# Kernel optimization log

Hardware: AMD Instinct MI355X
Metric: run time of the kernel (lower is better)

## Reference

```python
import jax, jax.numpy as jnp
import numpy as np

N, E, D_IN, D_H, G = 50000, 800000, 300, 128, 128


def gat_conv(x, src, dst, W, att_src, att_dst, bias):
    # PyG GATConv, heads=1, concat, negative_slope=0.2, self-loops already appended.
    h = x @ W                              # [N, F]
    a_s = h @ att_src                      # [N]
    a_d = h @ att_dst                      # [N]
    e = jax.nn.leaky_relu(a_s[src] + a_d[dst], 0.2)   # [E+N]
    m = jax.ops.segment_max(e, dst, num_segments=h.shape[0])
    ex = jnp.exp(e - m[dst])
    denom = jax.ops.segment_sum(ex, dst, num_segments=h.shape[0])
    alpha = ex / denom[dst]                # softmax over in-edges of each dst
    out = jax.ops.segment_sum(alpha[:, None] * h[src], dst, num_segments=h.shape[0])
    return out + bias


def setup_inputs() -> dict:
    key = jax.random.key(0)
    ks = jax.random.split(key, 12)
    x = jax.random.normal(ks[0], (N, D_IN), dtype=jnp.float32)
    edge_index = jax.random.randint(ks[1], (2, E), 0, N)
    batch = jnp.sort(jax.random.randint(ks[2], (N,), 0, G))
    pos = jax.random.randint(ks[3], (N,), 0, 2).astype(bool)
    s = 0.05
    W1 = jax.random.normal(ks[4], (D_IN, D_H), dtype=jnp.float32) * s
    as1 = jax.random.normal(ks[5], (D_H,), dtype=jnp.float32) * s
    ad1 = jax.random.normal(ks[6], (D_H,), dtype=jnp.float32) * s
    b1 = jnp.zeros((D_H,), dtype=jnp.float32)
    W2 = jax.random.normal(ks[7], (D_H, D_H), dtype=jnp.float32) * s
    as2 = jax.random.normal(ks[8], (D_H,), dtype=jnp.float32) * s
    ad2 = jax.random.normal(ks[9], (D_H,), dtype=jnp.float32) * s
    b2 = jnp.zeros((D_H,), dtype=jnp.float32)
    Wfc = jax.random.normal(ks[10], (D_H, 1), dtype=jnp.float32) * s
    bfc = jnp.zeros((1,), dtype=jnp.float32)
    return {"x": x, "edge_index": edge_index, "batch": batch, "pos": pos,
            "num_graphs": G, "W1": W1, "as1": as1, "ad1": ad1, "b1": b1,
            "W2": W2, "as2": as2, "ad2": ad2, "b2": b2, "Wfc": Wfc, "bfc": bfc}


def reference(x, edge_index, batch, pos, num_graphs, W1, as1, ad1, b1,
              W2, as2, ad2, b2, Wfc, bfc):
    n = x.shape[0]
    loop = jnp.arange(n)
    src = jnp.concatenate([edge_index[0], loop])
    dst = jnp.concatenate([edge_index[1], loop])
    h = gat_conv(x, src, dst, W1, as1, ad1, b1)
    h = jax.nn.gelu(h, approximate=False)
    # dropout is identity in eval mode
    h = gat_conv(h, src, dst, W2, as2, ad2, b2)   # [N, 128]
    # masked per-graph mean: logits[g] = mean over nodes with batch==g and pos
    w = pos.astype(h.dtype)                       # [N]
    sums = jax.ops.segment_sum(h * w[:, None], batch, num_segments=num_graphs)
    cnt = jax.ops.segment_sum(w, batch, num_segments=num_graphs)
    logits = sums / jnp.maximum(cnt, 1.0)[:, None]          # [G, 128]
    scores = (jax.nn.gelu(logits, approximate=False) @ Wfc + bfc).reshape(-1, num_graphs)
    return scores, logits
```

## Files before the change

### kernel.cpp

```cpp
#include <hip/hip_runtime.h>
#include <math.h>

#define NN 50000
#define EE 800000
#define DIN 300
#define DH 128
#define NG 128
#define RSIZE 6250

typedef __attribute__((ext_vector_type(8))) short short8;
typedef __attribute__((ext_vector_type(4))) float floatx4;

__device__ __forceinline__ float gelu_exact(float x) {
  return 0.5f * x * (1.0f + erff(x * 0.7071067811865476f));
}

__device__ __forceinline__ void split_bf16(float v, unsigned short& hi, unsigned short& lo) {
  unsigned int u = __float_as_uint(v);
  hi = (unsigned short)(u >> 16);
  float fh = __uint_as_float((unsigned int)hi << 16);
  lo = (unsigned short)(__float_as_uint(v - fh) >> 16);
}

__device__ __forceinline__ unsigned short f2bf_rne(float x) {
  unsigned int u = __float_as_uint(x);
  unsigned int r = (u + 0x7FFFu + ((u >> 16) & 1u)) >> 16;
  return (unsigned short)r;
}

__device__ __forceinline__ float bf_lo(unsigned u) { return __uint_as_float(u << 16); }
__device__ __forceinline__ float bf_hi(unsigned u) { return __uint_as_float(u & 0xFFFF0000u); }

__device__ __forceinline__ void async_ld16(void* lds, const void* g) {
  __builtin_amdgcn_global_load_lds(
      (const __attribute__((address_space(1))) unsigned int*)(unsigned long long)g,
      (__attribute__((address_space(3))) unsigned int*)(unsigned int)(unsigned long long)lds,
      16, 0, 0);
}


__global__ __launch_bounds__(256) void count_part_kernel(const int* __restrict__ ei,
                                                         int* __restrict__ deg,
                                                         int blocksPerRange) {
  const int r = blockIdx.x & 7;
  const int t = blockIdx.x >> 3;
  const int lo = r * RSIZE, hi = lo + RSIZE;
  const int total = EE + NN;
  const int step = blocksPerRange * 256;
  for (int e0 = t * 256; e0 < total; e0 += step) {
    int e = e0 + threadIdx.x;
    if (e < total) {
      int d = (e < EE) ? ei[EE + e] : (e - EE);
      if (d >= lo && d < hi) atomicAdd(&deg[d], 1);
    }
  }
}

__global__ __launch_bounds__(1024) void scan_part_kernel(const int* __restrict__ deg,
                                                         int* __restrict__ rowptr,
                                                         int* __restrict__ bsum) {
  __shared__ int wsum[16];
  const int tid = threadIdx.x;
  const int lane = tid & 63;
  const int wid = tid >> 6;
  int idx = blockIdx.x * 1024 + tid;
  int v = (idx < NN) ? deg[idx] : 0;
  int x = v;
#pragma unroll
  for (int d = 1; d < 64; d <<= 1) {
    int y = __shfl_up(x, d, 64);
    if (lane >= d) x += y;
  }
  if (lane == 63) wsum[wid] = x;
  __syncthreads();
  if (wid == 0) {
    int s = (lane < 16) ? wsum[lane] : 0;
#pragma unroll
    for (int d = 1; d < 16; d <<= 1) {
      int y = __shfl_up(s, d, 64);
      if (lane >= d) s += y;
    }
    if (lane < 16) wsum[lane] = s;
  }
  __syncthreads();
  int woff = (wid > 0) ? wsum[wid - 1] : 0;
  int incl = x + woff;
  if (idx < NN) rowptr[idx] = incl - v;
  if (tid == 1023) bsum[blockIdx.x] = incl;
}

__global__ __launch_bounds__(256) void scan_add_kernel(int* __restrict__ rowptr,
                                                       const int* __restrict__ bsum,
                                                       int* __restrict__ cursor, int nb) {
  __shared__ int boff_s[64];
  const int tid = threadIdx.x;
  if (tid < 64) {
    int lane = tid;
    int v = (lane < nb) ? bsum[lane] : 0;
    int x = v;
#pragma unroll
    for (int d = 1; d < 64; d <<= 1) {
      int y = __shfl_up(x, d, 64);
      if (lane >= d) x += y;
    }
    if (lane < nb) boff_s[lane] = x - v;
    if (lane == nb - 1) boff_s[nb] = x;
  }
  __syncthreads();
  int i = blockIdx.x * 256 + tid;
  if (i < NN) {
    int r = rowptr[i] + boff_s[i >> 10];
    rowptr[i] = r;
    cursor[i] = r;
  } else if (i == NN) {
    rowptr[NN] = boff_s[nb];
  }
}

__global__ __launch_bounds__(256) void scatter_part_kernel(const int* __restrict__ ei,
                                                           int* __restrict__ cursor,
                                                           int* __restrict__ colA,
                                                           int blocksPerRange) {
  const int r = blockIdx.x & 7;
  const int t = blockIdx.x >> 3;
  const int lo = r * RSIZE, hi = lo + RSIZE;
  const int total = EE + NN;
  const int step = blocksPerRange * 256;
  for (int e0 = t * 256; e0 < total; e0 += step) {
    int e = e0 + threadIdx.x;
    if (e < total) {
      int d = (e < EE) ? ei[EE + e] : (e - EE);
      if (d >= lo && d < hi) {
        int s = (e < EE) ? ei[e] : d;
        int p = atomicAdd(&cursor[d], 1);
        colA[p] = s;
      }
    }
  }
}


__global__ __launch_bounds__(256) void convert_bt2_kernel(
    const float* __restrict__ B1, unsigned short* __restrict__ B1h,
    unsigned short* __restrict__ B1l, int K1, int Kp1, int nblk1,
    const float* __restrict__ B2, unsigned short* __restrict__ B2h,
    unsigned short* __restrict__ B2l, int K2, int Kp2) {
  const float* B;
  unsigned short *Bh, *Bl;
  int K, Kpad, i;
  if ((int)blockIdx.x < nblk1) {
    B = B1; Bh = B1h; Bl = B1l; K = K1; Kpad = Kp1;
    i = blockIdx.x * 256 + threadIdx.x;
  } else {
    B = B2; Bh = B2h; Bl = B2l; K = K2; Kpad = Kp2;
    i = (blockIdx.x - nblk1) * 256 + threadIdx.x;
  }
  int n = i / Kpad, k = i % Kpad;
  if (n >= 128) return;
  float v = (k < K) ? B[(long)k * 128 + n] : 0.f;
  unsigned short h, l;
  split_bf16(v, h, l);
  Bh[(long)n * Kpad + k] = h;
  Bl[(long)n * Kpad + k] = l;
}


__global__ __launch_bounds__(256) void gemm_mfma_kernel(
    const float* __restrict__ A,
    const unsigned short* __restrict__ Bth, const unsigned short* __restrict__ Btl,
    unsigned short* __restrict__ C, int M, int K, int Kpad,
    const float* __restrict__ avs, const float* __restrict__ avd,
    float* __restrict__ aS, float* __restrict__ aD) {
  __shared__ __align__(16) unsigned short Bls[2][2][128 * 32];

  const int tid = threadIdx.x;
  const int lane = tid & 63;
  const int w = tid >> 6;
  const int q = lane >> 4;
  const int m16 = lane & 15;
  const int row0 = blockIdx.x * 64;
  const int myrow = row0 + w * 16 + m16;
  const bool rok = myrow < M;
  const long abase = (long)myrow * K;

  const int rl = lane >> 2, qq0 = lane & 3;
  const int nb0 = w * 16 + rl;
  const int nb1 = 64 + w * 16 + rl;
  const long boff0 = (long)nb0 * Kpad + (long)((qq0 ^ ((nb0 >> 1) & 3)) * 8);
  const long boff1 = (long)nb1 * Kpad + (long)((qq0 ^ ((nb1 >> 1) & 3)) * 8);

  floatx4 acc[8];
#pragma unroll
  for (int i = 0; i < 8; i++) acc[i] = (floatx4)(0.f);

  const int nsteps = Kpad / 32;

  float4 vA0, vA1, nA0, nA1;
  nA0 = nA1 = make_float4(0.f, 0.f, 0.f, 0.f);

  auto stageB = [&](int s, int nb) {
    const int k0 = s * 32;
    async_ld16(&Bls[nb][0][(w * 16) * 32], Bth + boff0 + k0);
    async_ld16(&Bls[nb][0][(64 + w * 16) * 32], Bth + boff1 + k0);
    async_ld16(&Bls[nb][1][(w * 16) * 32], Btl + boff0 + k0);
    async_ld16(&Bls[nb][1][(64 + w * 16) * 32], Btl + boff1 + k0);
  };
  auto loadA = [&](int s, float4& x0, float4& x1) {
    const int k0 = s * 32 + q * 8;
    x0 = make_float4(0.f, 0.f, 0.f, 0.f);
    x1 = x0;
    if (rok) {
      if (k0 + 4 <= K) x0 = *(const float4*)&A[abase + k0];
      if (k0 + 8 <= K) x1 = *(const float4*)&A[abase + k0 + 4];
    }
  };

  stageB(0, 0);
  loadA(0, vA0, vA1);
  __syncthreads();

  for (int s = 0; s < nsteps; s++) {
    const int cur = s & 1;
    if (s + 1 < nsteps) {
      stageB(s + 1, 1 ^ cur);
      loadA(s + 1, nA0, nA1);
    }
    float av[8] = {vA0.x, vA0.y, vA0.z, vA0.w, vA1.x, vA1.y, vA1.z, vA1.w};
    union {
      unsigned u[4];
      short8 s8;
    } Uh, Ul;
#pragma unroll
    for (int i = 0; i < 4; i++) {
      unsigned short ha, la, hb, lb;
      split_bf16(av[2 * i], ha, la);
      split_bf16(av[2 * i + 1], hb, lb);
      Uh.u[i] = (unsigned)ha | ((unsigned)hb << 16);
      Ul.u[i] = (unsigned)la | ((unsigned)lb << 16);
    }
    short8 afh = Uh.s8, afl = Ul.s8;
#pragma unroll
    for (int ct = 0; ct < 8; ct++) {
      int n = ct * 16 + m16;
      int qv = (q ^ ((n >> 1) & 3)) * 8;
      short8 bfh = *(const short8*)&Bls[cur][0][n * 32 + qv];
      short8 bfl = *(const short8*)&Bls[cur][1][n * 32 + qv];
      acc[ct] = __builtin_amdgcn_mfma_f32_16x16x32_bf16(afh, bfh, acc[ct], 0, 0, 0);
      acc[ct] = __builtin_amdgcn_mfma_f32_16x16x32_bf16(afh, bfl, acc[ct], 0, 0, 0);
      acc[ct] = __builtin_amdgcn_mfma_f32_16x16x32_bf16(afl, bfh, acc[ct], 0, 0, 0);
    }
    vA0 = nA0;
    vA1 = nA1;
    __syncthreads();
  }

  float avs_r[8], avd_r[8];
#pragma unroll
  for (int ct = 0; ct < 8; ct++) {
    avs_r[ct] = avs[ct * 16 + m16];
    avd_r[ct] = avd[ct * 16 + m16];
  }
#pragma unroll
  for (int reg = 0; reg < 4; reg++) {
    int grow = row0 + w * 16 + q * 4 + reg;
    bool ok = grow < M;
    float ps = 0.f, pd = 0.f;
#pragma unroll
    for (int ct = 0; ct < 8; ct++) {
      float c = acc[ct][reg];
      if (ok) C[(long)grow * 128 + ct * 16 + m16] = f2bf_rne(c);
      ps = fmaf(c, avs_r[ct], ps);
      pd = fmaf(c, avd_r[ct], pd);
    }
#pragma unroll
    for (int d = 1; d < 16; d <<= 1) {
      ps += __shfl_xor(ps, d, 64);
      pd += __shfl_xor(pd, d, 64);
    }
    if (m16 == 0 && ok) {
      aS[grow] = ps;
      aD[grow] = pd;
    }
  }
}


__global__ __launch_bounds__(256) void aggregate_kernel(const int* __restrict__ rowptr,
                                                        const int* __restrict__ colA,
                                                        const float* __restrict__ aS,
                                                        const float* __restrict__ aD,
                                                        const unsigned short* __restrict__ Hb,
                                                        const float* __restrict__ bias,
                                                        float* __restrict__ out,
                                                        int apply_gelu) {
  const int lane = threadIdx.x & 63;
  const int dst = blockIdx.x * 4 + (threadIdx.x >> 6);
  if (dst >= NN) return;
  const int start = rowptr[dst];
  const int end = rowptr[dst + 1];
  const int deg = end - start;
  const float ad = aD[dst];
  const int qg = lane >> 4;
  const int fl = lane & 15;

  float a0 = 0.f, a1 = 0.f, a2 = 0.f, a3 = 0.f;
  float a4 = 0.f, a5 = 0.f, a6 = 0.f, a7 = 0.f;

  auto gather8 = [&](int sj0, float wj0, int sj1, float wj1) {
    uint4 u0 = *(const uint4*)&Hb[(long)sj0 * DH + fl * 8];
    uint4 u1 = *(const uint4*)&Hb[(long)sj1 * DH + fl * 8];
    a0 = fmaf(wj0, bf_lo(u0.x), a0);
    a1 = fmaf(wj0, bf_hi(u0.x), a1);
    a2 = fmaf(wj0, bf_lo(u0.y), a2);
    a3 = fmaf(wj0, bf_hi(u0.y), a3);
    a4 = fmaf(wj0, bf_lo(u0.z), a4);
    a5 = fmaf(wj0, bf_hi(u0.z), a5);
    a6 = fmaf(wj0, bf_lo(u0.w), a6);
    a7 = fmaf(wj0, bf_hi(u0.w), a7);
    a0 = fmaf(wj1, bf_lo(u1.x), a0);
    a1 = fmaf(wj1, bf_hi(u1.x), a1);
    a2 = fmaf(wj1, bf_lo(u1.y), a2);
    a3 = fmaf(wj1, bf_hi(u1.y), a3);
    a4 = fmaf(wj1, bf_lo(u1.z), a4);
    a5 = fmaf(wj1, bf_hi(u1.z), a5);
    a6 = fmaf(wj1, bf_lo(u1.w), a6);
    a7 = fmaf(wj1, bf_hi(u1.w), a7);
  };

  if (deg <= 64) {
    int src = 0;
    float e = -__builtin_inff();
    if (lane < deg) {
      src = colA[start + lane];
      float v = aS[src] + ad;
      e = (v > 0.f) ? v : 0.2f * v;
    }
    float mx = e;
#pragma unroll
    for (int d = 1; d < 64; d <<= 1) mx = fmaxf(mx, __shfl_xor(mx, d, 64));
    float ew = (lane < deg) ? expf(e - mx) : 0.f;
    float ss = ew;
#pragma unroll
    for (int d = 1; d < 64; d <<= 1) ss += __shfl_xor(ss, d, 64);
    float wgt = ew * (1.f / ss);
    for (int j = 0; j < deg; j += 8) {
      int i0 = j + qg;
      int i1 = j + 4 + qg;
      int sj0 = __shfl(src, i0 & 63, 64);
      float wj0 = __shfl(wgt, i0 & 63, 64);
      if (i0 >= deg) wj0 = 0.f;
      int sj1 = __shfl(src, i1 & 63, 64);
      float wj1 = __shfl(wgt, i1 & 63, 64);
      if (i1 >= deg) wj1 = 0.f;
      gather8(sj0, wj0, sj1, wj1);
    }
  } else {
    float m = -__builtin_inff(), ssum = 0.f;
    for (int c0 = start; c0 < end; c0 += 64) {
      int i = c0 + lane;
      float e = -__builtin_inff();
      if (i < end) {
        int s = colA[i];
        float v = aS[s] + ad;
        e = (v > 0.f) ? v : 0.2f * v;
      }
      float cm = e;
#pragma unroll
      for (int d = 1; d < 64; d <<= 1) cm = fmaxf(cm, __shfl_xor(cm, d, 64));
      float ce = (i < end) ? expf(e - cm) : 0.f;
      float cs = ce;
#pragma unroll
      for (int d = 1; d < 64; d <<= 1) cs += __shfl_xor(cs, d, 64);
      float nm = fmaxf(m, cm);
      ssum = ssum * expf(m - nm) + cs * expf(cm - nm);
      m = nm;
    }
    float inv = 1.f / ssum;
    for (int c0 = start; c0 < end; c0 += 64) {
      int i = c0 + lane;
      int src = 0;
      float wgt = 0.f;
      if (i < end) {
        src = colA[i];
        float v = aS[src] + ad;
        float e = (v > 0.f) ? v : 0.2f * v;
        wgt = expf(e - m) * inv;
      }
      int lim = min(64, end - c0);
      for (int j = 0; j < lim; j += 8) {
        int i0 = j + qg;
        int i1 = j + 4 + qg;
        int sj0 = __shfl(src, i0 & 63, 64);
        float wj0 = __shfl(wgt, i0 & 63, 64);
        if (i0 >= lim) wj0 = 0.f;
        int sj1 = __shfl(src, i1 & 63, 64);
        float wj1 = __shfl(wgt, i1 & 63, 64);
        if (i1 >= lim) wj1 = 0.f;
        gather8(sj0, wj0, sj1, wj1);
      }
    }
  }

#pragma unroll
  for (int d = 16; d <= 32; d <<= 1) {
    a0 += __shfl_xor(a0, d, 64);
    a1 += __shfl_xor(a1, d, 64);
    a2 += __shfl_xor(a2, d, 64);
    a3 += __shfl_xor(a3, d, 64);
    a4 += __shfl_xor(a4, d, 64);
    a5 += __shfl_xor(a5, d, 64);
    a6 += __shfl_xor(a6, d, 64);
    a7 += __shfl_xor(a7, d, 64);
  }

  if (qg == 0) {
    float4 b0 = *(const float4*)&bias[fl * 8];
    float4 b1 = *(const float4*)&bias[fl * 8 + 4];
    float r0 = a0 + b0.x, r1 = a1 + b0.y, r2 = a2 + b0.z, r3 = a3 + b0.w;
    float r4 = a4 + b1.x, r5 = a5 + b1.y, r6 = a6 + b1.z, r7 = a7 + b1.w;
    if (apply_gelu) {
      r0 = gelu_exact(r0); r1 = gelu_exact(r1);
      r2 = gelu_exact(r2); r3 = gelu_exact(r3);
      r4 = gelu_exact(r4); r5 = gelu_exact(r5);
      r6 = gelu_exact(r6); r7 = gelu_exact(r7);
    }
    *(float4*)&out[(long)dst * DH + fl * 8] = make_float4(r0, r1, r2, r3);
    *(float4*)&out[(long)dst * DH + fl * 8 + 4] = make_float4(r4, r5, r6, r7);
  }
}


__global__ __launch_bounds__(128) void pool_kernel(const float* __restrict__ H,
                                                   const int* __restrict__ batch,
                                                   const int* __restrict__ pos,
                                                   float* __restrict__ sums,
                                                   float* __restrict__ cnt) {
  const int CH = 64;
  int n0 = blockIdx.x * CH;
  int n1 = min(n0 + CH, NN);
  int f = threadIdx.x;
  float acc = 0.f, c = 0.f;
  int g = batch[n0];
  for (int n = n0; n < n1; n += 4) {
    float h0 = H[(long)(n + 0) * DH + f];
    float h1 = H[(long)(n + 1) * DH + f];
    float h2 = H[(long)(n + 2) * DH + f];
    float h3 = H[(long)(n + 3) * DH + f];
    int g0 = batch[n + 0], g1 = batch[n + 1], g2 = batch[n + 2], g3 = batch[n + 3];
    int p0 = pos[n + 0], p1 = pos[n + 1], p2 = pos[n + 2], p3 = pos[n + 3];
    float hv[4] = {h0, h1, h2, h3};
    int gv[4] = {g0, g1, g2, g3};
    int pv[4] = {p0, p1, p2, p3};
#pragma unroll
    for (int i = 0; i < 4; i++) {
      if (gv[i] != g) {
        atomicAdd(&sums[g * DH + f], acc);
        if (f == 0) atomicAdd(&cnt[g], c);
        acc = 0.f; c = 0.f; g = gv[i];
      }
      if (pv[i]) {
        acc += hv[i];
        c += 1.f;
      }
    }
  }
  atomicAdd(&sums[g * DH + f], acc);
  if (f == 0) atomicAdd(&cnt[g], c);
}


__global__ __launch_bounds__(128) void head_kernel(const float* __restrict__ sums,
                                                   const float* __restrict__ cnt,
                                                   const float* __restrict__ Wfc,
                                                   const float* __restrict__ bfc,
                                                   float* __restrict__ out) {
  int g = blockIdx.x;
  int f = threadIdx.x;
  float c = fmaxf(cnt[g], 1.f);
  float logit = sums[g * DH + f] / c;
  out[NG + g * DH + f] = logit;
  float gl = gelu_exact(logit) * Wfc[f];
  __shared__ float red[2];
#pragma unroll
  for (int d = 1; d < 64; d <<= 1) gl += __shfl_xor(gl, d, 64);
  int lane = f & 63, w = f >> 6;
  if (lane == 0) red[w] = gl;
  __syncthreads();
  if (f == 0) out[g] = red[0] + red[1] + bfc[0];
}


extern "C" void kernel_launch(void* const* d_in, const int* in_sizes, int n_in,
                              void* d_out, int out_size, void* d_ws, size_t ws_size,
                              hipStream_t stream) {
  const float* x   = (const float*)d_in[0];
  const int* ei    = (const int*)d_in[1];
  const int* batch = (const int*)d_in[2];
  const int* pos   = (const int*)d_in[3];
  const float* W1  = (const float*)d_in[5];
  const float* as1 = (const float*)d_in[6];
  const float* ad1 = (const float*)d_in[7];
  const float* b1  = (const float*)d_in[8];
  const float* W2  = (const float*)d_in[9];
  const float* as2 = (const float*)d_in[10];
  const float* ad2 = (const float*)d_in[11];
  const float* b2  = (const float*)d_in[12];
  const float* Wfc = (const float*)d_in[13];
  const float* bfc = (const float*)d_in[14];
  float* out = (float*)d_out;

  const int KP1 = 320;
  const int KP2 = 128;
  const int NB_SCAN = (NN + 1023) / 1024;
  const int BPR = 416;

  char* ws = (char*)d_ws;
  size_t off = 0;
  auto nxt = [&](size_t b) -> void* {
    size_t p = off;
    off += (b + 255) & ~(size_t)255;
    return (void*)(ws + p);
  };
  int* rowptr = (int*)nxt((NN + 1) * sizeof(int));
  int* cursor = (int*)nxt(NN * sizeof(int));
  int* colA   = (int*)nxt((size_t)(EE + NN) * sizeof(int));
  int* bsum   = (int*)nxt((NB_SCAN + 1) * sizeof(int));
  float* aS   = (float*)nxt((size_t)2 * NN * sizeof(float));
  float* aD   = aS + NN;
  unsigned short* bufAb = (unsigned short*)nxt((size_t)NN * DH * sizeof(short));
  float* bufB = (float*)nxt((size_t)NN * DH * sizeof(float));
  float* sums = (float*)nxt((size_t)(NG * DH + NG) * sizeof(float));
  float* cnt  = sums + NG * DH;
  unsigned short* Bt1h = (unsigned short*)nxt((size_t)128 * KP1 * sizeof(short));
  unsigned short* Bt1l = (unsigned short*)nxt((size_t)128 * KP1 * sizeof(short));
  unsigned short* Bt2h = (unsigned short*)nxt((size_t)128 * KP2 * sizeof(short));
  unsigned short* Bt2l = (unsigned short*)nxt((size_t)128 * KP2 * sizeof(short));

  hipMemsetAsync(cursor, 0, NN * sizeof(int), stream);
  hipMemsetAsync(sums, 0, (NG * DH + NG) * sizeof(float), stream);

  const int cb1 = (128 * KP1 + 255) / 256;
  const int cb2 = (128 * KP2 + 255) / 256;
  convert_bt2_kernel<<<cb1 + cb2, 256, 0, stream>>>(W1, Bt1h, Bt1l, DIN, KP1, cb1,
                                                    W2, Bt2h, Bt2l, DH, KP2);

  count_part_kernel<<<8 * BPR, 256, 0, stream>>>(ei, cursor, BPR);
  scan_part_kernel<<<NB_SCAN, 1024, 0, stream>>>(cursor, rowptr, bsum);
  scan_add_kernel<<<(NN + 1 + 255) / 256, 256, 0, stream>>>(rowptr, bsum, cursor, NB_SCAN);
  scatter_part_kernel<<<8 * BPR, 256, 0, stream>>>(ei, cursor, colA, BPR);

  const int gblocks = (NN + 63) / 64;
  gemm_mfma_kernel<<<gblocks, 256, 0, stream>>>(x, Bt1h, Bt1l, bufAb, NN, DIN, KP1,
                                                as1, ad1, aS, aD);
  aggregate_kernel<<<(NN + 3) / 4, 256, 0, stream>>>(rowptr, colA, aS, aD, bufAb, b1, bufB, 1);
  gemm_mfma_kernel<<<gblocks, 256, 0, stream>>>(bufB, Bt2h, Bt2l, bufAb, NN, DH, KP2,
                                                as2, ad2, aS, aD);
  aggregate_kernel<<<(NN + 3) / 4, 256, 0, stream>>>(rowptr, colA, aS, aD, bufAb, b2, bufB, 0);
  pool_kernel<<<(NN + 63) / 64, 128, 0, stream>>>(bufB, batch, pos, sums, cnt);
  head_kernel<<<NG, 128, 0, stream>>>(sums, cnt, Wfc, bfc, out);
}
```

Measured before the change: 331.8 us.

## Pack two destination nodes per wavefront in aggregation for low-degree pairs

Each 64-lane wavefront now handles two destination nodes, one per 32-lane half, when both have degree at most 32. Each half computes softmax over up to 32 edges and gathers with two edge groups of 16 lanes. Otherwise the wave falls back to processing the two nodes sequentially with the original full-wave path. This removes idle lanes for typical low-degree nodes and halves the block count, at the cost of divergence and serialized fallback for waves containing a high-degree node.

```diff
diff --git a/kernel.cpp b/kernel.cpp
--- a/kernel.cpp
+++ b/kernel.cpp
@@ -294,138 +294,227 @@
                                                         float* __restrict__ out,
                                                         int apply_gelu) {
   const int lane = threadIdx.x & 63;
-  const int dst = blockIdx.x * 4 + (threadIdx.x >> 6);
-  if (dst >= NN) return;
+  const int w = threadIdx.x >> 6;
+  const int pair = blockIdx.x * 8 + w * 2;
+  const int half = lane >> 5;
+  const int hl = lane & 31;
+  const int dst = pair + half;
   const int start = rowptr[dst];
   const int end = rowptr[dst + 1];
   const int deg = end - start;
-  const float ad = aD[dst];
+
+  unsigned long long bal = __ballot(deg <= 32);
+  if (bal == ~0ull) {
+    const float ad = aD[dst];
+    int src = 0;
+    float e = -__builtin_inff();
+    if (hl < deg) {
+      src = colA[start + hl];
+      float v = aS[src] + ad;
+      e = (v > 0.f) ? v : 0.2f * v;
+    }
+    float mx = e;
+#pragma unroll
+    for (int d = 1; d < 32; d <<= 1) mx = fmaxf(mx, __shfl_xor(mx, d, 32));
+    float ew = (hl < deg) ? expf(e - mx) : 0.f;
+    float ss = ew;
+#pragma unroll
+    for (int d = 1; d < 32; d <<= 1) ss += __shfl_xor(ss, d, 32);
+    float wgt = ew * (1.f / ss);
+
+    const int qg2 = hl >> 4;
+    const int fl = hl & 15;
+    const int base = half * 32;
+
+    float a0 = 0.f, a1 = 0.f, a2 = 0.f, a3 = 0.f;
+    float a4 = 0.f, a5 = 0.f, a6 = 0.f, a7 = 0.f;
+    for (int j = 0; j < deg; j += 4) {
+      int i0 = j + qg2;
+      int i1 = j + 2 + qg2;
+      int sj0 = __shfl(src, base + (i0 & 31), 64);
+      float wj0 = __shfl(wgt, base + (i0 & 31), 64);
+      if (i0 >= deg) wj0 = 0.f;
+      int sj1 = __shfl(src, base + (i1 & 31), 64);
+      float wj1 = __shfl(wgt, base + (i1 & 31), 64);
+      if (i1 >= deg) wj1 = 0.f;
+      uint4 u0 = *(const uint4*)&Hb[(long)sj0 * DH + fl * 8];
+      uint4 u1 = *(const uint4*)&Hb[(long)sj1 * DH + fl * 8];
+      a0 = fmaf(wj0, bf_lo(u0.x), a0);
+      a1 = fmaf(wj0, bf_hi(u0.x), a1);
+      a2 = fmaf(wj0, bf_lo(u0.y), a2);
+      a3 = fmaf(wj0, bf_hi(u0.y), a3);
+      a4 = fmaf(wj0, bf_lo(u0.z), a4);
+      a5 = fmaf(wj0, bf_hi(u0.z), a5);
+      a6 = fmaf(wj0, bf_lo(u0.w), a6);
+      a7 = fmaf(wj0, bf_hi(u0.w), a7);
+      a0 = fmaf(wj1, bf_lo(u1.x), a0);
+      a1 = fmaf(wj1, bf_hi(u1.x), a1);
+      a2 = fmaf(wj1, bf_lo(u1.y), a2);
+      a3 = fmaf(wj1, bf_hi(u1.y), a3);
+      a4 = fmaf(wj1, bf_lo(u1.z), a4);
+      a5 = fmaf(wj1, bf_hi(u1.z), a5);
+      a6 = fmaf(wj1, bf_lo(u1.w), a6);
+      a7 = fmaf(wj1, bf_hi(u1.w), a7);
+    }
+    a0 += __shfl_xor(a0, 16, 64);
+    a1 += __shfl_xor(a1, 16, 64);
+    a2 += __shfl_xor(a2, 16, 64);
+    a3 += __shfl_xor(a3, 16, 64);
+    a4 += __shfl_xor(a4, 16, 64);
+    a5 += __shfl_xor(a5, 16, 64);
+    a6 += __shfl_xor(a6, 16, 64);
+    a7 += __shfl_xor(a7, 16, 64);
+
+    if (qg2 == 0) {
+      float4 b0 = *(const float4*)&bias[fl * 8];
+      float4 b1 = *(const float4*)&bias[fl * 8 + 4];
+      float r0 = a0 + b0.x, r1 = a1 + b0.y, r2 = a2 + b0.z, r3 = a3 + b0.w;
+      float r4 = a4 + b1.x, r5 = a5 + b1.y, r6 = a6 + b1.z, r7 = a7 + b1.w;
+      if (apply_gelu) {
+        r0 = gelu_exact(r0); r1 = gelu_exact(r1);
+        r2 = gelu_exact(r2); r3 = gelu_exact(r3);
+        r4 = gelu_exact(r4); r5 = gelu_exact(r5);
+        r6 = gelu_exact(r6); r7 = gelu_exact(r7);
+      }
+      *(float4*)&out[(long)dst * DH + fl * 8] = make_float4(r0, r1, r2, r3);
+      *(float4*)&out[(long)dst * DH + fl * 8 + 4] = make_float4(r4, r5, r6, r7);
+    }
+    return;
+  }
+
   const int qg = lane >> 4;
   const int fl = lane & 15;
-
-  float a0 = 0.f, a1 = 0.f, a2 = 0.f, a3 = 0.f;
-  float a4 = 0.f, a5 = 0.f, a6 = 0.f, a7 = 0.f;
-
-  auto gather8 = [&](int sj0, float wj0, int sj1, float wj1) {
-    uint4 u0 = *(const uint4*)&Hb[(long)sj0 * DH + fl * 8];
-    uint4 u1 = *(const uint4*)&Hb[(long)sj1 * DH + fl * 8];
-    a0 = fmaf(wj0, bf_lo(u0.x), a0);
-    a1 = fmaf(wj0, bf_hi(u0.x), a1);
-    a2 = fmaf(wj0, bf_lo(u0.y), a2);
-    a3 = fmaf(wj0, bf_hi(u0.y), a3);
-    a4 = fmaf(wj0, bf_lo(u0.z), a4);
-    a5 = fmaf(wj0, bf_hi(u0.z), a5);
-    a6 = fmaf(wj0, bf_lo(u0.w), a6);
-    a7 = fmaf(wj0, bf_hi(u0.w), a7);
-    a0 = fmaf(wj1, bf_lo(u1.x), a0);
-    a1 = fmaf(wj1, bf_hi(u1.x), a1);
-    a2 = fmaf(wj1, bf_lo(u1.y), a2);
-    a3 = fmaf(wj1, bf_hi(u1.y), a3);
-    a4 = fmaf(wj1, bf_lo(u1.z), a4);
-    a5 = fmaf(wj1, bf_hi(u1.z), a5);
-    a6 = fmaf(wj1, bf_lo(u1.w), a6);
-    a7 = fmaf(wj1, bf_hi(u1.w), a7);
-  };
-
-  if (deg <= 64) {
-    int src = 0;
-    float e = -__builtin_inff();
-    if (lane < deg) {
-      src = colA[start + lane];
-      float v = aS[src] + ad;
-      e = (v > 0.f) ? v : 0.2f * v;
-    }
-    float mx = e;
-#pragma unroll
-    for (int d = 1; d < 64; d <<= 1) mx = fmaxf(mx, __shfl_xor(mx, d, 64));
-    float ew = (lane < deg) ? expf(e - mx) : 0.f;
-    float ss = ew;
-#pragma unroll
-    for (int d = 1; d < 64; d <<= 1) ss += __shfl_xor(ss, d, 64);
-    float wgt = ew * (1.f / ss);
-    for (int j = 0; j < deg; j += 8) {
-      int i0 = j + qg;
-      int i1 = j + 4 + qg;
-      int sj0 = __shfl(src, i0 & 63, 64);
-      float wj0 = __shfl(wgt, i0 & 63, 64);
-      if (i0 >= deg) wj0 = 0.f;
-      int sj1 = __shfl(src, i1 & 63, 64);
-      float wj1 = __shfl(wgt, i1 & 63, 64);
-      if (i1 >= deg) wj1 = 0.f;
-      gather8(sj0, wj0, sj1, wj1);
-    }
-  } else {
-    float m = -__builtin_inff(), ssum = 0.f;
-    for (int c0 = start; c0 < end; c0 += 64) {
-      int i = c0 + lane;
+  for (int t = 0; t < 2; t++) {
+    const int d2 = pair + t;
+    const int st = rowptr[d2];
+    const int en = rowptr[d2 + 1];
+    const int dg = en - st;
+    const float ad = aD[d2];
+
+    float a0 = 0.f, a1 = 0.f, a2 = 0.f, a3 = 0.f;
+    float a4 = 0.f, a5 = 0.f, a6 = 0.f, a7 = 0.f;
+
+    auto gather8 = [&](int sj0, float wj0, int sj1, float wj1) {
+      uint4 u0 = *(const uint4*)&Hb[(long)sj0 * DH + fl * 8];
+      uint4 u1 = *(const uint4*)&Hb[(long)sj1 * DH + fl * 8];
+      a0 = fmaf(wj0, bf_lo(u0.x), a0);
+      a1 = fmaf(wj0, bf_hi(u0.x), a1);
+      a2 = fmaf(wj0, bf_lo(u0.y), a2);
+      a3 = fmaf(wj0, bf_hi(u0.y), a3);
+      a4 = fmaf(wj0, bf_lo(u0.z), a4);
+      a5 = fmaf(wj0, bf_hi(u0.z), a5);
+      a6 = fmaf(wj0, bf_lo(u0.w), a6);
+      a7 = fmaf(wj0, bf_hi(u0.w), a7);
+      a0 = fmaf(wj1, bf_lo(u1.x), a0);
+      a1 = fmaf(wj1, bf_hi(u1.x), a1);
+      a2 = fmaf(wj1, bf_lo(u1.y), a2);
+      a3 = fmaf(wj1, bf_hi(u1.y), a3);
+      a4 = fmaf(wj1, bf_lo(u1.z), a4);
+      a5 = fmaf(wj1, bf_hi(u1.z), a5);
+      a6 = fmaf(wj1, bf_lo(u1.w), a6);
+      a7 = fmaf(wj1, bf_hi(u1.w), a7);
+    };
+
+    if (dg <= 64) {
+      int src = 0;
       float e = -__builtin_inff();
-      if (i < end) {
-        int s = colA[i];
-        float v = aS[s] + ad;
+      if (lane < dg) {
+        src = colA[st + lane];
+        float v = aS[src] + ad;
         e = (v > 0.f) ? v : 0.2f * v;
       }
-      float cm = e;
-#pragma unroll
-      for (int d = 1; d < 64; d <<= 1) cm = fmaxf(cm, __shfl_xor(cm, d, 64));
-      float ce = (i < end) ? expf(e - cm) : 0.f;
-      float cs = ce;
-#pragma unroll
-      for (int d = 1; d < 64; d <<= 1) cs += __shfl_xor(cs, d, 64);
-      float nm = fmaxf(m, cm);
-      ssum = ssum * expf(m - nm) + cs * expf(cm - nm);
-      m = nm;
-    }
-    float inv = 1.f / ssum;
-    for (int c0 = start; c0 < end; c0 += 64) {
-      int i = c0 + lane;
-      int src = 0;
-      float wgt = 0.f;
-      if (i < end) {
-        src = colA[i];
-        float v = aS[src] + ad;
-        float e = (v > 0.f) ? v : 0.2f * v;
-        wgt = expf(e - m) * inv;
-      }
-      int lim = min(64, end - c0);
-      for (int j = 0; j < lim; j += 8) {
+      float mx = e;
+#pragma unroll
+      for (int d = 1; d < 64; d <<= 1) mx = fmaxf(mx, __shfl_xor(mx, d, 64));
+      float ew = (lane < dg) ? expf(e - mx) : 0.f;
+      float ss = ew;
+#pragma unroll
+      for (int d = 1; d < 64; d <<= 1) ss += __shfl_xor(ss, d, 64);
+      float wgt = ew * (1.f / ss);
+      for (int j = 0; j < dg; j += 8) {
         int i0 = j + qg;
         int i1 = j + 4 + qg;
         int sj0 = __shfl(src, i0 & 63, 64);
         float wj0 = __shfl(wgt, i0 & 63, 64);
-        if (i0 >= lim) wj0 = 0.f;
+        if (i0 >= dg) wj0 = 0.f;
         int sj1 = __shfl(src, i1 & 63, 64);
         float wj1 = __shfl(wgt, i1 & 63, 64);
-        if (i1 >= lim) wj1 = 0.f;
+        if (i1 >= dg) wj1 = 0.f;
         gather8(sj0, wj0, sj1, wj1);
       }
-    }
-  }
-
-#pragma unroll
-  for (int d = 16; d <= 32; d <<= 1) {
-    a0 += __shfl_xor(a0, d, 64);
-    a1 += __shfl_xor(a1, d, 64);
-    a2 += __shfl_xor(a2, d, 64);
-    a3 += __shfl_xor(a3, d, 64);
-    a4 += __shfl_xor(a4, d, 64);
-    a5 += __shfl_xor(a5, d, 64);
-    a6 += __shfl_xor(a6, d, 64);
-    a7 += __shfl_xor(a7, d, 64);
-  }
-
-  if (qg == 0) {
-    float4 b0 = *(const float4*)&bias[fl * 8];
-    float4 b1 = *(const float4*)&bias[fl * 8 + 4];
-    float r0 = a0 + b0.x, r1 = a1 + b0.y, r2 = a2 + b0.z, r3 = a3 + b0.w;
-    float r4 = a4 + b1.x, r5 = a5 + b1.y, r6 = a6 + b1.z, r7 = a7 + b1.w;
-    if (apply_gelu) {
-      r0 = gelu_exact(r0); r1 = gelu_exact(r1);
-      r2 = gelu_exact(r2); r3 = gelu_exact(r3);
-      r4 = gelu_exact(r4); r5 = gelu_exact(r5);
-      r6 = gelu_exact(r6); r7 = gelu_exact(r7);
-    }
-    *(float4*)&out[(long)dst * DH + fl * 8] = make_float4(r0, r1, r2, r3);
-    *(float4*)&out[(long)dst * DH + fl * 8 + 4] = make_float4(r4, r5, r6, r7);
+    } else {
+      float m = -__builtin_inff(), ssum = 0.f;
+      for (int c0 = st; c0 < en; c0 += 64) {
+        int i = c0 + lane;
+        float e = -__builtin_inff();
+        if (i < en) {
+          int s = colA[i];
+          float v = aS[s] + ad;
+          e = (v > 0.f) ? v : 0.2f * v;
+        }
+        float cm = e;
+#pragma unroll
+        for (int d = 1; d < 64; d <<= 1) cm = fmaxf(cm, __shfl_xor(cm, d, 64));
+        float ce = (i < en) ? expf(e - cm) : 0.f;
+        float cs = ce;
+#pragma unroll
+        for (int d = 1; d < 64; d <<= 1) cs += __shfl_xor(cs, d, 64);
+        float nm = fmaxf(m, cm);
+        ssum = ssum * expf(m - nm) + cs * expf(cm - nm);
+        m = nm;
+      }
+      float inv = 1.f / ssum;
+      for (int c0 = st; c0 < en; c0 += 64) {
+        int i = c0 + lane;
+        int src = 0;
+        float wgt = 0.f;
+        if (i < en) {
+          src = colA[i];
+          float v = aS[src] + ad;
+          float e = (v > 0.f) ? v : 0.2f * v;
+          wgt = expf(e - m) * inv;
+        }
+        int lim = min(64, en - c0);
+        for (int j = 0; j < lim; j += 8) {
+          int i0 = j + qg;
+          int i1 = j + 4 + qg;
+          int sj0 = __shfl(src, i0 & 63, 64);
+          float wj0 = __shfl(wgt, i0 & 63, 64);
+          if (i0 >= lim) wj0 = 0.f;
+          int sj1 = __shfl(src, i1 & 63, 64);
+          float wj1 = __shfl(wgt, i1 & 63, 64);
+          if (i1 >= lim) wj1 = 0.f;
+          gather8(sj0, wj0, sj1, wj1);
+        }
+      }
+    }
+
+#pragma unroll
+    for (int d = 16; d <= 32; d <<= 1) {
+      a0 += __shfl_xor(a0, d, 64);
+      a1 += __shfl_xor(a1, d, 64);
+      a2 += __shfl_xor(a2, d, 64);
+      a3 += __shfl_xor(a3, d, 64);
+      a4 += __shfl_xor(a4, d, 64);
+      a5 += __shfl_xor(a5, d, 64);
+      a6 += __shfl_xor(a6, d, 64);
+      a7 += __shfl_xor(a7, d, 64);
+    }
+
+    if (qg == 0) {
+      float4 b0 = *(const float4*)&bias[fl * 8];
+      float4 b1 = *(const float4*)&bias[fl * 8 + 4];
+      float r0 = a0 + b0.x, r1 = a1 + b0.y, r2 = a2 + b0.z, r3 = a3 + b0.w;
+      float r4 = a4 + b1.x, r5 = a5 + b1.y, r6 = a6 + b1.z, r7 = a7 + b1.w;
+      if (apply_gelu) {
+        r0 = gelu_exact(r0); r1 = gelu_exact(r1);
+        r2 = gelu_exact(r2); r3 = gelu_exact(r3);
+        r4 = gelu_exact(r4); r5 = gelu_exact(r5);
+        r6 = gelu_exact(r6); r7 = gelu_exact(r7);
+      }
+      *(float4*)&out[(long)d2 * DH + fl * 8] = make_float4(r0, r1, r2, r3);
+      *(float4*)&out[(long)d2 * DH + fl * 8 + 4] = make_float4(r4, r5, r6, r7);
+    }
   }
 }
 
@@ -552,10 +641,10 @@
   const int gblocks = (NN + 63) / 64;
   gemm_mfma_kernel<<<gblocks, 256, 0, stream>>>(x, Bt1h, Bt1l, bufAb, NN, DIN, KP1,
                                                 as1, ad1, aS, aD);
-  aggregate_kernel<<<(NN + 3) / 4, 256, 0, stream>>>(rowptr, colA, aS, aD, bufAb, b1, bufB, 1);
+  aggregate_kernel<<<NN / 8, 256, 0, stream>>>(rowptr, colA, aS, aD, bufAb, b1, bufB, 1);
   gemm_mfma_kernel<<<gblocks, 256, 0, stream>>>(bufB, Bt2h, Bt2l, bufAb, NN, DH, KP2,
                                                 as2, ad2, aS, aD);
-  aggregate_kernel<<<(NN + 3) / 4, 256, 0, stream>>>(rowptr, colA, aS, aD, bufAb, b2, bufB, 0);
+  aggregate_kernel<<<NN / 8, 256, 0, stream>>>(rowptr, colA, aS, aD, bufAb, b2, bufB, 0);
   pool_kernel<<<(NN + 63) / 64, 128, 0, stream>>>(bufB, batch, pos, sums, cnt);
   head_kernel<<<NG, 128, 0, stream>>>(sums, cnt, Wfc, bfc, out);
 }
```

Result: faster. 321.8 us (-3.0%).
